# Kernel optimization log

Hardware: AMD Instinct MI355X
Metric: run time of the kernel (lower is better)

## Reference

```python
import jax, jax.numpy as jnp
import numpy as np

N_NODES = 30000
N_EDGES = 480000
IN_FEATS = 256
H_FEATS = 128
HEADS = 4
OUT_DIM = 128
NEG_SLOPE = 0.2  # PyG GATConv default leaky_relu slope


def gat_conv(x, src, dst, W, att_src, att_dst, bias, concat):
    """PyG-style GATConv (eval mode, self-loops already in src/dst).
    x: [N, Fin]; W: [Fin, H*C]; att_src/att_dst: [H, C]; bias: [H*C] or [C].
    """
    N = x.shape[0]
    H, C = att_src.shape
    h = (x @ W).reshape(N, H, C)                       # [N, H, C]
    a_src = jnp.einsum('nhc,hc->nh', h, att_src)       # [N, H]
    a_dst = jnp.einsum('nhc,hc->nh', h, att_dst)
    e = jax.nn.leaky_relu(a_src[src] + a_dst[dst], NEG_SLOPE)  # [E, H]
    # segment softmax over incoming edges of each dst node
    m = jax.ops.segment_max(e, dst, num_segments=N)    # [N, H]
    m = jnp.where(jnp.isfinite(m), m, 0.0)
    ex = jnp.exp(e - m[dst])
    denom = jax.ops.segment_sum(ex, dst, num_segments=N)
    alpha = ex / denom[dst]                            # [E, H]
    msg = alpha[:, :, None] * h[src]                   # [E, H, C]
    out = jax.ops.segment_sum(msg, dst, num_segments=N)  # [N, H, C]
    if concat:
        out = out.reshape(N, H * C)
    else:
        out = out.mean(axis=1)
    return out + bias


def setup_inputs() -> dict:
    key = jax.random.key(0)
    ks = jax.random.split(key, 12)
    s = 0.05
    x = jax.random.normal(ks[0], (N_NODES, IN_FEATS), dtype=jnp.float32)
    edge_index = jax.random.randint(ks[1], (2, N_EDGES), 0, N_NODES, dtype=jnp.int64)
    W1 = jax.random.normal(ks[2], (IN_FEATS, HEADS * H_FEATS), dtype=jnp.float32) * s
    att_src1 = jax.random.normal(ks[3], (HEADS, H_FEATS), dtype=jnp.float32) * s
    att_dst1 = jax.random.normal(ks[4], (HEADS, H_FEATS), dtype=jnp.float32) * s
    b1 = jnp.zeros((HEADS * H_FEATS,), dtype=jnp.float32)
    W2 = jax.random.normal(ks[5], (HEADS * H_FEATS, HEADS * H_FEATS), dtype=jnp.float32) * s
    att_src2 = jax.random.normal(ks[6], (HEADS, H_FEATS), dtype=jnp.float32) * s
    att_dst2 = jax.random.normal(ks[7], (HEADS, H_FEATS), dtype=jnp.float32) * s
    b2 = jnp.zeros((HEADS * H_FEATS,), dtype=jnp.float32)
    W3 = jax.random.normal(ks[8], (HEADS * H_FEATS, OUT_DIM), dtype=jnp.float32) * s
    att_src3 = jax.random.normal(ks[9], (1, OUT_DIM), dtype=jnp.float32) * s
    att_dst3 = jax.random.normal(ks[10], (1, OUT_DIM), dtype=jnp.float32) * s
    b3 = jnp.zeros((OUT_DIM,), dtype=jnp.float32)
    return {"x": x, "edge_index": edge_index,
            "W1": W1, "att_src1": att_src1, "att_dst1": att_dst1, "b1": b1,
            "W2": W2, "att_src2": att_src2, "att_dst2": att_dst2, "b2": b2,
            "W3": W3, "att_src3": att_src3, "att_dst3": att_dst3, "b3": b3}


def reference(x, edge_index, W1, att_src1, att_dst1, b1,
              W2, att_src2, att_dst2, b2, W3, att_src3, att_dst3, b3):
    # PyG GATConv adds self-loops by default
    loops = jnp.arange(N_NODES, dtype=edge_index.dtype)
    src = jnp.concatenate([edge_index[0], loops])
    dst = jnp.concatenate([edge_index[1], loops])
    h = gat_conv(x, src, dst, W1, att_src1, att_dst1, b1, concat=True)
    h = jax.nn.relu(h)  # dropout inactive in eval mode
    h = gat_conv(h, src, dst, W2, att_src2, att_dst2, b2, concat=True)
    h = jax.nn.relu(h)
    out = gat_conv(h, src, dst, W3, att_src3, att_dst3, b3, concat=False)
    return out
```

## Files before the change

kernel.cpp:

```cpp
#include <hip/hip_runtime.h>


#define NEG_SLOPE 0.2f

typedef __attribute__((ext_vector_type(8))) short short8;
typedef __attribute__((ext_vector_type(4))) float floatx4;

static __device__ __forceinline__ unsigned short f2bf(float f) {
    unsigned u = __float_as_uint(f);
    u = u + 0x7FFFu + ((u >> 16) & 1u);
    return (unsigned short)(u >> 16);
}
static __device__ __forceinline__ float bf2f_lo(unsigned u) {
    return __uint_as_float(u << 16);
}
static __device__ __forceinline__ float bf2f_hi(unsigned u) {
    return __uint_as_float(u & 0xFFFF0000u);
}

static __device__ __forceinline__ void async_copy16(const void* g, void* l) {
    __builtin_amdgcn_global_load_lds(
        (const __attribute__((address_space(1))) unsigned int*)g,
        (__attribute__((address_space(3))) unsigned int*)l, 16, 0, 0);
}


__global__ __launch_bounds__(256)
void prep_hist_kernel(const float* __restrict__ x, unsigned short* __restrict__ x_bf,
                      const float* __restrict__ W1, unsigned short* __restrict__ W1T,
                      const float* __restrict__ W2, unsigned short* __restrict__ W2T,
                      const float* __restrict__ W3, unsigned short* __restrict__ W3T,
                      const int* __restrict__ ei, int* cursor, int n4, int E) {
    int i = blockIdx.x * 256 + threadIdx.x;
    if (i < n4) {
        float4 v = ((const float4*)x)[i];
        ushort4 o;
        o.x = f2bf(v.x); o.y = f2bf(v.y); o.z = f2bf(v.z); o.w = f2bf(v.w);
        ((ushort4*)x_bf)[i] = o;
        return;
    }
    int j = i - n4;
    if (j < 256 * 512) {
        int k = j >> 9, n = j & 511;
        W1T[(size_t)n * 256 + k] = f2bf(W1[j]);
        return;
    }
    j -= 256 * 512;
    if (j < 512 * 512) {
        int k = j >> 9, n = j & 511;
        W2T[(size_t)n * 512 + k] = f2bf(W2[j]);
        return;
    }
    j -= 512 * 512;
    if (j < 512 * 128) {
        int k = j >> 7, n = j & 127;
        W3T[(size_t)n * 512 + k] = f2bf(W3[j]);
        return;
    }
    j -= 512 * 128;
    if (j < E) atomicAdd(&cursor[ei[E + j]], 1);
}


__global__ __launch_bounds__(1024)
void scan_bsum_kernel(const int* __restrict__ cursor, int* __restrict__ bsum, int N) {
    __shared__ int wsum[16];
    int tid = threadIdx.x, lane = tid & 63, w = tid >> 6;
    int i = blockIdx.x * 1024 + tid;
    int v = (i < N) ? cursor[i] : 0;
    #pragma unroll
    for (int off = 32; off; off >>= 1) v += __shfl_xor(v, off, 64);
    if (lane == 0) wsum[w] = v;
    __syncthreads();
    if (tid == 0) {
        int t = 0;
        #pragma unroll
        for (int k = 0; k < 16; ++k) t += wsum[k];
        bsum[blockIdx.x] = t;
    }
}

__global__ __launch_bounds__(1024)
void scan_final_kernel(int* __restrict__ cursor, const int* __restrict__ bsum,
                       int* __restrict__ row_ptr, int N, int NB) {
    __shared__ int wsum[16];
    __shared__ int boff_sh;
    int tid = threadIdx.x, lane = tid & 63, w = tid >> 6;
    if (w == 0) {
        int bv = (lane < NB) ? bsum[lane] : 0;
        int bx = bv;
        #pragma unroll
        for (int off = 1; off < 64; off <<= 1) {
            int t = __shfl_up(bx, off, 64);
            if (lane >= off) bx += t;
        }
        if (lane == blockIdx.x) boff_sh = bx - bv;
        if (blockIdx.x == 0 && lane == 63) row_ptr[N] = bx + N;
    }
    int i = blockIdx.x * 1024 + tid;
    int v = (i < N) ? cursor[i] : 0;
    int x = v;
    #pragma unroll
    for (int off = 1; off < 64; off <<= 1) {
        int t = __shfl_up(x, off, 64);
        if (lane >= off) x += t;
    }
    if (lane == 63) wsum[w] = x;
    __syncthreads();
    if (w == 0 && lane < 16) {
        int y = wsum[lane];
        #pragma unroll
        for (int off = 1; off < 16; off <<= 1) {
            int t = __shfl_up(y, off, 64);
            if (lane >= off) y += t;
        }
        wsum[lane] = y;
    }
    __syncthreads();
    int woff = (w == 0) ? 0 : wsum[w - 1];
    int ex = boff_sh + woff + x - v + i;
    if (i < N) { row_ptr[i] = ex; cursor[i] = ex; }
}

__global__ __launch_bounds__(256)
void scatter_kernel(const int* __restrict__ ei, int* cursor,
                    int* __restrict__ csr_src, int E, int N) {
    int i = blockIdx.x * 256 + threadIdx.x;
    if (i < E) {
        int s = ei[i], d = ei[E + i];
        int pos = atomicAdd(&cursor[d], 1);
        csr_src[pos] = s;
    } else if (i < E + N) {
        int n = i - E;
        int pos = atomicAdd(&cursor[n], 1);
        csr_src[pos] = n;
    }
}


template<int TM, int TN>
__global__ __launch_bounds__(512)
void mfma_gemm_kernel(const unsigned short* __restrict__ A,
                      const unsigned short* __restrict__ BT,
                      unsigned short* __restrict__ C,
                      const float* __restrict__ att_src,
                      const float* __restrict__ att_dst,
                      float* __restrict__ a_srcO, float* __restrict__ a_dstO,
                      int H, int M, int Nn, int K) {
    constexpr int NH = TN / 128;
    __shared__ unsigned short buf[(TM + TN) * 64];
    __shared__ float psum[TN / 64][TM];
    __shared__ float pdsum[TN / 64][TM];
    const int tid = threadIdx.x;
    const int m0 = blockIdx.y * TM;
    const int n0 = blockIdx.x * TN;
    const int head_base = blockIdx.x * NH;
    const int lane = tid & 63, wave = tid >> 6;
    const int wm = (wave & (TM / 64 - 1)) * 64;
    const int wn = (wave / (TM / 64)) * 64;
    const int quad = lane >> 4, rr = lane & 15;

    const int srow = lane >> 3;
    const int sseg = (lane & 7) ^ srow;
    const unsigned short* gptr[6];
    unsigned short* lptr[6];
    #pragma unroll
    for (int j = 0; j < 6; ++j) {
        int base_row = wave * 48 + j * 8;
        lptr[j] = buf + base_row * 64;
        if (base_row < TM) {
            int gr = min(m0 + base_row + srow, M - 1);
            gptr[j] = A + (size_t)gr * K;
        } else {
            int gr = n0 + (base_row - TM) + srow;
            gptr[j] = BT + (size_t)gr * K;
        }
    }

    floatx4 acc[4][4] = {};

    for (int k0 = 0; k0 < K; k0 += 64) {
        #pragma unroll
        for (int j = 0; j < 6; ++j)
            async_copy16(gptr[j] + k0 + sseg * 8, lptr[j]);
        __syncthreads();

        #pragma unroll
        for (int k32 = 0; k32 < 2; ++k32) {
            short8 af[4], bf[4];
            #pragma unroll
            for (int mi = 0; mi < 4; ++mi) {
                int row = wm + mi * 16 + rr;
                int phys = (k32 * 4 + quad) ^ (rr & 7);
                af[mi] = *(const short8*)(buf + row * 64 + phys * 8);
            }
            #pragma unroll
            for (int ni = 0; ni < 4; ++ni) {
                int row = TM + wn + ni * 16 + rr;
                int phys = (k32 * 4 + quad) ^ (rr & 7);
                bf[ni] = *(const short8*)(buf + row * 64 + phys * 8);
            }
            #pragma unroll
            for (int mi = 0; mi < 4; ++mi)
                #pragma unroll
                for (int ni = 0; ni < 4; ++ni)
                    acc[mi][ni] = __builtin_amdgcn_mfma_f32_16x16x32_bf16(
                        af[mi], bf[ni], acc[mi][ni], 0, 0, 0);
        }
        __syncthreads();
    }

    #pragma unroll
    for (int mi = 0; mi < 4; ++mi) {
        #pragma unroll
        for (int ni = 0; ni < 4; ++ni) {
            int col = n0 + wn + ni * 16 + rr;
            #pragma unroll
            for (int r = 0; r < 4; ++r) {
                int row = m0 + wm + mi * 16 + quad * 4 + r;
                if (row < M) C[(size_t)row * Nn + col] = f2bf(acc[mi][ni][r]);
            }
        }
    }

    float ats[4], atd[4];
    #pragma unroll
    for (int ni = 0; ni < 4; ++ni) {
        int cc = wn + ni * 16;
        int h = head_base + (cc >> 7);
        int c = (cc + rr) & 127;
        ats[ni] = att_src[h * 128 + c];
        atd[ni] = att_dst[h * 128 + c];
    }
    const int wg = wn >> 6;
    #pragma unroll
    for (int mi = 0; mi < 4; ++mi) {
        #pragma unroll
        for (int r = 0; r < 4; ++r) {
            float ps = 0.f, pd = 0.f;
            #pragma unroll
            for (int ni = 0; ni < 4; ++ni) {
                ps += ats[ni] * acc[mi][ni][r];
                pd += atd[ni] * acc[mi][ni][r];
            }
            #pragma unroll
            for (int off = 1; off < 16; off <<= 1) {
                ps += __shfl_xor(ps, off, 64);
                pd += __shfl_xor(pd, off, 64);
            }
            if (rr == 0) {
                int row = wm + mi * 16 + quad * 4 + r;
                psum[wg][row] = ps;
                pdsum[wg][row] = pd;
            }
        }
    }
    __syncthreads();
    if (tid < NH * TM) {
        int h = tid / TM, r = tid % TM;
        int gr = m0 + r;
        if (gr < M) {
            a_srcO[(size_t)gr * H + head_base + h] = psum[2 * h][r] + psum[2 * h + 1][r];
            a_dstO[(size_t)gr * H + head_base + h] = pdsum[2 * h][r] + pdsum[2 * h + 1][r];
        }
    }
}


template<int F, int H, bool RELU, bool BF16OUT>
__global__ __launch_bounds__(256)
void agg_kernel(const unsigned* __restrict__ hfeat, const float* __restrict__ a_src,
                const float* __restrict__ a_dst, const int* __restrict__ row_ptr,
                const int* __restrict__ csr_src, const float* __restrict__ bias,
                void* __restrict__ out_v, int N) {
    constexpr int UPL = F / 128;
    constexpr int RU = F / 2;
    const int wave = threadIdx.x >> 6, lane = threadIdx.x & 63;
    const int n = blockIdx.x * 4 + wave;
    if (n >= N) return;
    const int begin = __builtin_amdgcn_readfirstlane(row_ptr[n]);
    const int deg = __builtin_amdgcn_readfirstlane(row_ptr[n + 1]) - begin;
    const int myh = (2 * UPL * lane) / 128;
    const float adst = a_dst[n * H + myh];

    float acc[2 * UPL];
    #pragma unroll
    for (int j = 0; j < 2 * UPL; ++j) acc[j] = 0.f;
    float dacc = 0.f;

    unsigned u0[UPL], u1[UPL], u2[UPL], u3[UPL];
    float av0 = 0.f, av1 = 0.f, av2 = 0.f, av3 = 0.f;

#define LOADSLOT(idx, U, AV)                                              \
    {                                                                     \
        int s_ = __builtin_amdgcn_readfirstlane(csr_src[begin + (idx)]);  \
        if (UPL == 4) {                                                   \
            uint4 t_ = ((const uint4*)(hfeat + (size_t)s_ * RU))[lane];   \
            U[0] = t_.x; U[1] = t_.y; U[2] = t_.z; U[3] = t_.w;           \
        } else {                                                          \
            U[0] = hfeat[(size_t)s_ * RU + lane];                         \
        }                                                                 \
        AV = a_src[s_ * H + myh];                                         \
    }

#define CONSUME(U, AV)                                                    \
    {                                                                     \
        float e_ = AV + adst;                                             \
        e_ = e_ > 0.f ? e_ : NEG_SLOPE * e_;                              \
        float ex_ = __expf(e_);                                           \
        dacc += ex_;                                                      \
        _Pragma("unroll")                                                 \
        for (int q_ = 0; q_ < UPL; ++q_) {                                \
            acc[2 * q_]     += ex_ * bf2f_lo(U[q_]);                      \
            acc[2 * q_ + 1] += ex_ * bf2f_hi(U[q_]);                      \
        }                                                                 \
    }

    LOADSLOT(0, u0, av0);
    if (deg > 1) LOADSLOT(1, u1, av1);
    if (deg > 2) LOADSLOT(2, u2, av2);
    if (deg > 3) LOADSLOT(3, u3, av3);
    int i = 0;
    for (; i + 8 <= deg; i += 4) {
        CONSUME(u0, av0); LOADSLOT(i + 4, u0, av0);
        CONSUME(u1, av1); LOADSLOT(i + 5, u1, av1);
        CONSUME(u2, av2); LOADSLOT(i + 6, u2, av2);
        CONSUME(u3, av3); LOADSLOT(i + 7, u3, av3);
    }
    int rem = deg - i;
    CONSUME(u0, av0); if (rem > 4) LOADSLOT(i + 4, u0, av0);
    if (rem > 1) { CONSUME(u1, av1); if (rem > 5) LOADSLOT(i + 5, u1, av1); }
    if (rem > 2) { CONSUME(u2, av2); if (rem > 6) LOADSLOT(i + 6, u2, av2); }
    if (rem > 3) CONSUME(u3, av3);
    if (rem > 4) CONSUME(u0, av0);
    if (rem > 5) CONSUME(u1, av1);
    if (rem > 6) CONSUME(u2, av2);
#undef LOADSLOT
#undef CONSUME

    float inv = 1.f / dacc;
    const int cb = 2 * UPL * lane;
    if (BF16OUT) {
        unsigned pk[UPL];
        #pragma unroll
        for (int q = 0; q < UPL; ++q) {
            float v0 = acc[2 * q] * inv + bias[cb + 2 * q];
            float v1 = acc[2 * q + 1] * inv + bias[cb + 2 * q + 1];
            if (RELU) { v0 = fmaxf(v0, 0.f); v1 = fmaxf(v1, 0.f); }
            pk[q] = (unsigned)f2bf(v0) | ((unsigned)f2bf(v1) << 16);
        }
        if (UPL == 4) {
            uint4 t; t.x = pk[0]; t.y = pk[1]; t.z = pk[2]; t.w = pk[3];
            ((uint4*)((unsigned*)out_v + (size_t)n * RU))[lane] = t;
        } else {
            ((unsigned*)out_v)[(size_t)n * RU + lane] = pk[0];
        }
    } else {
        #pragma unroll
        for (int q = 0; q < UPL; ++q) {
            float v0 = acc[2 * q] * inv + bias[cb + 2 * q];
            float v1 = acc[2 * q + 1] * inv + bias[cb + 2 * q + 1];
            if (RELU) { v0 = fmaxf(v0, 0.f); v1 = fmaxf(v1, 0.f); }
            float2 o; o.x = v0; o.y = v1;
            ((float2*)((float*)out_v + (size_t)n * F))[UPL * lane + q] = o;
        }
    }
}


extern "C" void kernel_launch(void* const* d_in, const int* in_sizes, int n_in,
                              void* d_out, int out_size, void* d_ws, size_t ws_size,
                              hipStream_t stream) {
    const float* x        = (const float*)d_in[0];
    const int*   ei       = (const int*)  d_in[1];
    const float* W1       = (const float*)d_in[2];
    const float* att_src1 = (const float*)d_in[3];
    const float* att_dst1 = (const float*)d_in[4];
    const float* b1       = (const float*)d_in[5];
    const float* W2       = (const float*)d_in[6];
    const float* att_src2 = (const float*)d_in[7];
    const float* att_dst2 = (const float*)d_in[8];
    const float* b2       = (const float*)d_in[9];
    const float* W3       = (const float*)d_in[10];
    const float* att_src3 = (const float*)d_in[11];
    const float* att_dst3 = (const float*)d_in[12];
    const float* b3       = (const float*)d_in[13];

    const int IN_FEATS = 256;
    const int N = in_sizes[0] / IN_FEATS;
    const int E = in_sizes[1] / 2;
    const int ET = E + N;
    const int NB = (N + 1023) / 1024;

    char* p = (char*)d_ws;
    unsigned short* h_bf    = (unsigned short*)p; p += (size_t)N * 512 * sizeof(unsigned short);
    unsigned short* act_bf  = (unsigned short*)p; p += (size_t)N * 512 * sizeof(unsigned short);
    unsigned short* x_bf    = (unsigned short*)p; p += (size_t)N * 256 * sizeof(unsigned short);
    float*          a_src   = (float*)p;          p += (size_t)N * 4 * sizeof(float);
    float*          a_dst   = (float*)p;          p += (size_t)N * 4 * sizeof(float);
    unsigned short* W1T     = (unsigned short*)p; p += (size_t)512 * 256 * sizeof(unsigned short);
    unsigned short* W2T     = (unsigned short*)p; p += (size_t)512 * 512 * sizeof(unsigned short);
    unsigned short* W3T     = (unsigned short*)p; p += (size_t)128 * 512 * sizeof(unsigned short);
    int*            row_ptr = (int*)p;            p += ((size_t)N + 16) * sizeof(int);
    int*            cursor  = (int*)p;            p += ((size_t)N + 16) * sizeof(int);
    int*            bsum    = (int*)p;            p += 64 * sizeof(int);
    int*            csr_src = (int*)p;            p += (size_t)ET * sizeof(int);

    hipMemsetAsync(cursor, 0, (size_t)N * sizeof(int), stream);
    {
        int n4 = N * 256 / 4;
        int total = n4 + 256 * 512 + 512 * 512 + 512 * 128 + E;
        prep_hist_kernel<<<(total + 255) / 256, 256, 0, stream>>>(
            x, x_bf, W1, W1T, W2, W2T, W3, W3T, ei, cursor, n4, E);
    }
    scan_bsum_kernel<<<NB, 1024, 0, stream>>>(cursor, bsum, N);
    scan_final_kernel<<<NB, 1024, 0, stream>>>(cursor, bsum, row_ptr, N, NB);
    scatter_kernel<<<(E + N + 255) / 256, 256, 0, stream>>>(ei, cursor, csr_src, E, N);

    const int MB128 = (N + 127) / 128;
    const int MB256 = (N + 255) / 256;
    const int NB4 = (N + 3) / 4;

    mfma_gemm_kernel<128, 256><<<dim3(2, MB128), 512, 0, stream>>>(x_bf, W1T, h_bf, att_src1, att_dst1, a_src, a_dst, 4, N, 512, 256);
    agg_kernel<512, 4, true, true><<<NB4, 256, 0, stream>>>((const unsigned*)h_bf, a_src, a_dst, row_ptr, csr_src, b1, act_bf, N);

    mfma_gemm_kernel<128, 256><<<dim3(2, MB128), 512, 0, stream>>>(act_bf, W2T, h_bf, att_src2, att_dst2, a_src, a_dst, 4, N, 512, 512);
    agg_kernel<512, 4, true, true><<<NB4, 256, 0, stream>>>((const unsigned*)h_bf, a_src, a_dst, row_ptr, csr_src, b2, act_bf, N);

    mfma_gemm_kernel<256, 128><<<dim3(1, MB256), 512, 0, stream>>>(act_bf, W3T, h_bf, att_src3, att_dst3, a_src, a_dst, 1, N, 128, 512);
    agg_kernel<128, 1, false, false><<<NB4, 256, 0, stream>>>((const unsigned*)h_bf, a_src, a_dst, row_ptr, csr_src, b3, d_out, N);
}
```

Measured before the change: 389.6 us.

## Split aggregation across feature slices and process multiple edges per wave

The aggregation kernel now splits each node's feature row into slices handled by separate blocks. Inside a wave, lanes are grouped so each group handles a different edge in parallel, then the groups are combined with xor shuffles. Attention logits are stored head-major so the per-slice a_src/a_dst gathers read one contiguous array. Loads and stores use nontemporal hints and the pipeline is double-buffered. This exposes more memory parallelism for low-degree nodes, at the cost of redundant index and logit loads per slice plus the shuffle reductions.

```diff
diff --git a/kernel.cpp b/kernel.cpp
--- a/kernel.cpp
+++ b/kernel.cpp
@@ -5,6 +5,7 @@
 
 typedef __attribute__((ext_vector_type(8))) short short8;
 typedef __attribute__((ext_vector_type(4))) float floatx4;
+typedef __attribute__((ext_vector_type(4))) unsigned uintx4;
 
 static __device__ __forceinline__ unsigned short f2bf(float f) {
     unsigned u = __float_as_uint(f);
@@ -260,109 +261,105 @@
         int h = tid / TM, r = tid % TM;
         int gr = m0 + r;
         if (gr < M) {
-            a_srcO[(size_t)gr * H + head_base + h] = psum[2 * h][r] + psum[2 * h + 1][r];
-            a_dstO[(size_t)gr * H + head_base + h] = pdsum[2 * h][r] + pdsum[2 * h + 1][r];
-        }
-    }
-}
-
-
-template<int F, int H, bool RELU, bool BF16OUT>
+            a_srcO[(size_t)(head_base + h) * M + gr] = psum[2 * h][r] + psum[2 * h + 1][r];
+            a_dstO[(size_t)(head_base + h) * M + gr] = pdsum[2 * h][r] + pdsum[2 * h + 1][r];
+        }
+    }
+}
+
+
+template<int F, int H, int NSLICE, bool RELU, bool BF16OUT>
 __global__ __launch_bounds__(256)
 void agg_kernel(const unsigned* __restrict__ hfeat, const float* __restrict__ a_src,
                 const float* __restrict__ a_dst, const int* __restrict__ row_ptr,
                 const int* __restrict__ csr_src, const float* __restrict__ bias,
                 void* __restrict__ out_v, int N) {
-    constexpr int UPL = F / 128;
     constexpr int RU = F / 2;
-    const int wave = threadIdx.x >> 6, lane = threadIdx.x & 63;
-    const int n = blockIdx.x * 4 + wave;
+    constexpr int SU = RU / NSLICE;
+    constexpr int GS = SU / 4;
+    constexpr int EPW = 64 / GS;
+    constexpr int FS = F / NSLICE;
+    const int lane = threadIdx.x & 63, wave = threadIdx.x >> 6;
+    const int s = blockIdx.x % NSLICE;
+    const int n = (blockIdx.x / NSLICE) * 4 + wave;
     if (n >= N) return;
     const int begin = __builtin_amdgcn_readfirstlane(row_ptr[n]);
-    const int deg = __builtin_amdgcn_readfirstlane(row_ptr[n + 1]) - begin;
-    const int myh = (2 * UPL * lane) / 128;
-    const float adst = a_dst[n * H + myh];
-
-    float acc[2 * UPL];
-    #pragma unroll
-    for (int j = 0; j < 2 * UPL; ++j) acc[j] = 0.f;
+    const int deg   = __builtin_amdgcn_readfirstlane(row_ptr[n + 1]) - begin;
+    const int g = lane / GS;
+    const int l = lane & (GS - 1);
+    const int h = (s * FS) / (F / H);
+    const float adst = a_dst[(size_t)h * N + n];
+    const unsigned* __restrict__ sbase = hfeat + (size_t)s * SU + l * 4;
+
+    float acc[8] = {};
     float dacc = 0.f;
 
-    unsigned u0[UPL], u1[UPL], u2[UPL], u3[UPL];
-    float av0 = 0.f, av1 = 0.f, av2 = 0.f, av3 = 0.f;
-
-#define LOADSLOT(idx, U, AV)                                              \
-    {                                                                     \
-        int s_ = __builtin_amdgcn_readfirstlane(csr_src[begin + (idx)]);  \
-        if (UPL == 4) {                                                   \
-            uint4 t_ = ((const uint4*)(hfeat + (size_t)s_ * RU))[lane];   \
-            U[0] = t_.x; U[1] = t_.y; U[2] = t_.z; U[3] = t_.w;           \
-        } else {                                                          \
-            U[0] = hfeat[(size_t)s_ * RU + lane];                         \
-        }                                                                 \
-        AV = a_src[s_ * H + myh];                                         \
-    }
-
-#define CONSUME(U, AV)                                                    \
-    {                                                                     \
-        float e_ = AV + adst;                                             \
-        e_ = e_ > 0.f ? e_ : NEG_SLOPE * e_;                              \
-        float ex_ = __expf(e_);                                           \
-        dacc += ex_;                                                      \
-        _Pragma("unroll")                                                 \
-        for (int q_ = 0; q_ < UPL; ++q_) {                                \
-            acc[2 * q_]     += ex_ * bf2f_lo(U[q_]);                      \
-            acc[2 * q_ + 1] += ex_ * bf2f_hi(U[q_]);                      \
-        }                                                                 \
-    }
-
-    LOADSLOT(0, u0, av0);
-    if (deg > 1) LOADSLOT(1, u1, av1);
-    if (deg > 2) LOADSLOT(2, u2, av2);
-    if (deg > 3) LOADSLOT(3, u3, av3);
-    int i = 0;
-    for (; i + 8 <= deg; i += 4) {
-        CONSUME(u0, av0); LOADSLOT(i + 4, u0, av0);
-        CONSUME(u1, av1); LOADSLOT(i + 5, u1, av1);
-        CONSUME(u2, av2); LOADSLOT(i + 6, u2, av2);
-        CONSUME(u3, av3); LOADSLOT(i + 7, u3, av3);
-    }
-    int rem = deg - i;
-    CONSUME(u0, av0); if (rem > 4) LOADSLOT(i + 4, u0, av0);
-    if (rem > 1) { CONSUME(u1, av1); if (rem > 5) LOADSLOT(i + 5, u1, av1); }
-    if (rem > 2) { CONSUME(u2, av2); if (rem > 6) LOADSLOT(i + 6, u2, av2); }
-    if (rem > 3) CONSUME(u3, av3);
-    if (rem > 4) CONSUME(u0, av0);
-    if (rem > 5) CONSUME(u1, av1);
-    if (rem > 6) CONSUME(u2, av2);
-#undef LOADSLOT
+    uintx4 u0, u1;
+    float av0 = 0.f, av1 = 0.f;
+
+#define LOADB(b, U, AV)                                                       \
+    {                                                                         \
+        int e_ = (b) * EPW + g;                                               \
+        int src_ = __builtin_nontemporal_load(                                \
+            csr_src + begin + (e_ < deg ? e_ : deg - 1));                     \
+        U = *(const uintx4*)(sbase + (size_t)src_ * RU);                      \
+        AV = a_src[(size_t)h * N + src_];                                     \
+    }
+
+#define CONSUME(b, U, AV)                                                     \
+    {                                                                         \
+        float e_ = AV + adst;                                                 \
+        e_ = e_ > 0.f ? e_ : NEG_SLOPE * e_;                                  \
+        float ex_ = ((b) * EPW + g < deg) ? __expf(e_) : 0.f;                 \
+        dacc += ex_;                                                          \
+        _Pragma("unroll")                                                     \
+        for (int q_ = 0; q_ < 4; ++q_) {                                      \
+            acc[2 * q_]     += ex_ * bf2f_lo(U[q_]);                          \
+            acc[2 * q_ + 1] += ex_ * bf2f_hi(U[q_]);                          \
+        }                                                                     \
+    }
+
+    const int nb = (deg + EPW - 1) / EPW;
+    LOADB(0, u0, av0);
+    int b = 0;
+    for (; b + 1 < nb; ++b) {
+        if (b & 1) { LOADB(b + 1, u0, av0); CONSUME(b, u1, av1); }
+        else       { LOADB(b + 1, u1, av1); CONSUME(b, u0, av0); }
+    }
+    if (b & 1) { CONSUME(b, u1, av1); }
+    else       { CONSUME(b, u0, av0); }
+#undef LOADB
 #undef CONSUME
 
-    float inv = 1.f / dacc;
-    const int cb = 2 * UPL * lane;
-    if (BF16OUT) {
-        unsigned pk[UPL];
-        #pragma unroll
-        for (int q = 0; q < UPL; ++q) {
-            float v0 = acc[2 * q] * inv + bias[cb + 2 * q];
-            float v1 = acc[2 * q + 1] * inv + bias[cb + 2 * q + 1];
-            if (RELU) { v0 = fmaxf(v0, 0.f); v1 = fmaxf(v1, 0.f); }
-            pk[q] = (unsigned)f2bf(v0) | ((unsigned)f2bf(v1) << 16);
-        }
-        if (UPL == 4) {
-            uint4 t; t.x = pk[0]; t.y = pk[1]; t.z = pk[2]; t.w = pk[3];
-            ((uint4*)((unsigned*)out_v + (size_t)n * RU))[lane] = t;
+    #pragma unroll
+    for (int off = GS; off < 64; off <<= 1) {
+        dacc += __shfl_xor(dacc, off, 64);
+        #pragma unroll
+        for (int q = 0; q < 8; ++q) acc[q] += __shfl_xor(acc[q], off, 64);
+    }
+
+    if (lane < GS) {
+        float inv = 1.f / dacc;
+        const int cb = s * FS + l * 8;
+        float v[8];
+        #pragma unroll
+        for (int j = 0; j < 8; ++j) {
+            float t = acc[j] * inv + bias[cb + j];
+            v[j] = RELU ? fmaxf(t, 0.f) : t;
+        }
+        if (BF16OUT) {
+            uintx4 pk;
+            #pragma unroll
+            for (int q = 0; q < 4; ++q)
+                pk[q] = (unsigned)f2bf(v[2 * q]) | ((unsigned)f2bf(v[2 * q + 1]) << 16);
+            __builtin_nontemporal_store(pk,
+                (uintx4*)((unsigned*)out_v + (size_t)n * RU + s * SU + l * 4));
         } else {
-            ((unsigned*)out_v)[(size_t)n * RU + lane] = pk[0];
-        }
-    } else {
-        #pragma unroll
-        for (int q = 0; q < UPL; ++q) {
-            float v0 = acc[2 * q] * inv + bias[cb + 2 * q];
-            float v1 = acc[2 * q + 1] * inv + bias[cb + 2 * q + 1];
-            if (RELU) { v0 = fmaxf(v0, 0.f); v1 = fmaxf(v1, 0.f); }
-            float2 o; o.x = v0; o.y = v1;
-            ((float2*)((float*)out_v + (size_t)n * F))[UPL * lane + q] = o;
+            floatx4 o0 = {v[0], v[1], v[2], v[3]};
+            floatx4 o1 = {v[4], v[5], v[6], v[7]};
+            float* dst = (float*)out_v + (size_t)n * F + cb;
+            __builtin_nontemporal_store(o0, (floatx4*)dst);
+            __builtin_nontemporal_store(o1, (floatx4*)(dst + 4));
         }
     }
 }
@@ -422,11 +419,11 @@
     const int NB4 = (N + 3) / 4;
 
     mfma_gemm_kernel<128, 256><<<dim3(2, MB128), 512, 0, stream>>>(x_bf, W1T, h_bf, att_src1, att_dst1, a_src, a_dst, 4, N, 512, 256);
-    agg_kernel<512, 4, true, true><<<NB4, 256, 0, stream>>>((const unsigned*)h_bf, a_src, a_dst, row_ptr, csr_src, b1, act_bf, N);
+    agg_kernel<512, 4, 8, true, true><<<8 * NB4, 256, 0, stream>>>((const unsigned*)h_bf, a_src, a_dst, row_ptr, csr_src, b1, act_bf, N);
 
     mfma_gemm_kernel<128, 256><<<dim3(2, MB128), 512, 0, stream>>>(act_bf, W2T, h_bf, att_src2, att_dst2, a_src, a_dst, 4, N, 512, 512);
-    agg_kernel<512, 4, true, true><<<NB4, 256, 0, stream>>>((const unsigned*)h_bf, a_src, a_dst, row_ptr, csr_src, b2, act_bf, N);
+    agg_kernel<512, 4, 8, true, true><<<8 * NB4, 256, 0, stream>>>((const unsigned*)h_bf, a_src, a_dst, row_ptr, csr_src, b2, act_bf, N);
 
     mfma_gemm_kernel<256, 128><<<dim3(1, MB256), 512, 0, stream>>>(act_bf, W3T, h_bf, att_src3, att_dst3, a_src, a_dst, 1, N, 128, 512);
-    agg_kernel<128, 1, false, false><<<NB4, 256, 0, stream>>>((const unsigned*)h_bf, a_src, a_dst, row_ptr, csr_src, b3, d_out, N);
-}
+    agg_kernel<128, 1, 2, false, false><<<2 * NB4, 256, 0, stream>>>((const unsigned*)h_bf, a_src, a_dst, row_ptr, csr_src, b3, d_out, N);
+}
```

Result: slower. 490.3 us (+25.8%).
